# Performance work log

Hardware: AMD Instinct MI355X
Metric: run time of the kernel (lower is better)

The kernel has to match this reference:

```python
import jax, jax.numpy as jnp
import numpy as np

D_MODEL = 1024
NUM_HEADS = 16
D_K = D_MODEL // NUM_HEADS
S, B = 2048, 2


def setup_inputs() -> dict:
    key = jax.random.key(0)
    ks = jax.random.split(key, 11)
    lim = 1.0 / np.sqrt(D_MODEL)
    def lin(kw, kb):
        W = jax.random.uniform(kw, (D_MODEL, D_MODEL), jnp.float32, -lim, lim)
        b = jax.random.uniform(kb, (D_MODEL,), jnp.float32, -lim, lim)
        return W, b
    Wq, bq = lin(ks[0], ks[1])
    Wk, bk = lin(ks[2], ks[3])
    Wv, bv = lin(ks[4], ks[5])
    Wo, bo = lin(ks[6], ks[7])
    q = jax.random.normal(ks[8], (S, B, D_MODEL), jnp.float32)
    k = jax.random.normal(ks[9], (S, B, D_MODEL), jnp.float32)
    v = jax.random.normal(ks[10], (S, B, D_MODEL), jnp.float32)
    return {"q": q, "k": k, "v": v,
            "Wq": Wq, "bq": bq, "Wk": Wk, "bk": bk,
            "Wv": Wv, "bv": bv, "Wo": Wo, "bo": bo}


def reference(q, k, v, Wq, bq, Wk, bk, Wv, bv, Wo, bo):
    s, b, _ = q.shape
    scale = np.sqrt(D_K).astype(np.float32)
    # torch Linear: x @ W.T + b
    def proj(x, W, bias):
        y = jnp.einsum('sbd,ed->sbe', x, W) + bias
        # [S,B,D] -> [B,H,S,d_k]
        return y.reshape(s, b, NUM_HEADS, D_K).transpose(1, 2, 0, 3)
    Q = proj(q, Wq, bq)
    K = proj(k, Wk, bk)
    V = proj(v, Wv, bv)
    scores = jnp.einsum('bhsd,bhtd->bhst', Q, K) / scale  # [B,H,S,S]
    attn = jax.nn.softmax(scores, axis=-1)
    ctx = jnp.einsum('bhst,bhtd->bhsd', attn, V)  # [B,H,S,d_k]
    ctx = ctx.transpose(2, 0, 1, 3).reshape(s, b, NUM_HEADS * D_K)
    return jnp.einsum('sbd,ed->sbe', ctx, Wo) + bo
```

## Files before the change

kernel.cpp:

```cpp
#include <hip/hip_runtime.h>
#include <stdint.h>

typedef __attribute__((ext_vector_type(8))) short short8;
typedef __attribute__((ext_vector_type(4))) float f32x4;
typedef __attribute__((ext_vector_type(16))) float f32x16;

#define MFMA16(a, b, c) __builtin_amdgcn_mfma_f32_16x16x32_bf16((a), (b), (c), 0, 0, 0)
#define MFMA32(a, b, c) __builtin_amdgcn_mfma_f32_32x32x16_bf16((a), (b), (c), 0, 0, 0)

__device__ inline unsigned short f2bf(float x) {
  unsigned u = __float_as_uint(x);
  u = (u + 0x7FFFu + ((u >> 16) & 1u)) >> 16;
  return (unsigned short)u;
}

__device__ inline void gload16(const unsigned short* g, unsigned short* l) {
  __builtin_amdgcn_global_load_lds(
      (const __attribute__((address_space(1))) unsigned int*)g,
      (__attribute__((address_space(3))) unsigned int*)l, 16, 0, 0);
}

__device__ inline short8 lds8(const unsigned short* base, int byteoff) {
  return *reinterpret_cast<const short8*>(reinterpret_cast<const char*>(base) + byteoff);
}

__device__ inline unsigned cvtpk(float lo, float hi) {
  unsigned r;
  asm("v_cvt_pk_bf16_f32 %0, %1, %2" : "=v"(r) : "v"(lo), "v"(hi));
  return r;
}
__device__ inline void plswap(unsigned& a, unsigned& b) {
  asm volatile("v_permlane32_swap_b32 %0, %1" : "+v"(a), "+v"(b));
}
__device__ inline float swapadd(float v) {
  float a = v, b;
  asm volatile("v_mov_b32 %1, %0\n\tv_permlane32_swap_b32 %0, %1" : "+v"(a), "=&v"(b));
  return a + b;
}

__device__ inline short8 mk8(unsigned a, unsigned b, unsigned c, unsigned d) {
  union { unsigned u[4]; short8 v; } x;
  x.u[0] = a; x.u[1] = b; x.u[2] = c; x.u[3] = d;
  return x.v;
}

__device__ inline int swz(int row, int chunk) {
  return row * 128 + (((chunk) ^ (row & 7)) << 4);
}

__device__ inline void exppack(const f32x16& sv, float& lsum, short8& paLo, short8& paHi) {
  float p[16];
#pragma unroll
  for (int i = 0; i < 16; ++i) p[i] = __builtin_amdgcn_exp2f(sv[i]);
  float q8[8];
#pragma unroll
  for (int i = 0; i < 8; ++i) q8[i] = p[2 * i] + p[2 * i + 1];
#pragma unroll
  for (int s2 = 4; s2 > 0; s2 >>= 1)
#pragma unroll
    for (int i = 0; i < s2; ++i) q8[i] += q8[i + s2];
  lsum += q8[0];
  unsigned w0 = cvtpk(p[0], p[1]), w1 = cvtpk(p[2], p[3]);
  unsigned w2 = cvtpk(p[4], p[5]), w3 = cvtpk(p[6], p[7]);
  plswap(w0, w2); plswap(w1, w3);
  unsigned w4 = cvtpk(p[8], p[9]), w5 = cvtpk(p[10], p[11]);
  unsigned w6 = cvtpk(p[12], p[13]), w7 = cvtpk(p[14], p[15]);
  plswap(w4, w6); plswap(w5, w7);
  paLo = mk8(w0, w1, w2, w3);
  paHi = mk8(w4, w5, w6, w7);
}

__global__ __launch_bounds__(256) void cvt_bf16x(const float* __restrict__ a0,
                                                 const float* __restrict__ a1,
                                                 const float* __restrict__ a2,
                                                 const float* __restrict__ a3,
                                                 unsigned short* __restrict__ d, int per) {
  int y = blockIdx.y;
  const float* s = (y == 0) ? a0 : (y == 1) ? a1 : (y == 2) ? a2 : a3;
  int i = (blockIdx.x * 256 + threadIdx.x) * 8;
  if (i >= per) return;
  float4 v0 = *reinterpret_cast<const float4*>(s + i);
  float4 v1 = *reinterpret_cast<const float4*>(s + i + 4);
  short8 o;
  o[0] = (short)f2bf(v0.x); o[1] = (short)f2bf(v0.y);
  o[2] = (short)f2bf(v0.z); o[3] = (short)f2bf(v0.w);
  o[4] = (short)f2bf(v1.x); o[5] = (short)f2bf(v1.y);
  o[6] = (short)f2bf(v1.z); o[7] = (short)f2bf(v1.w);
  *reinterpret_cast<short8*>(d + (size_t)y * per + i) = o;
}

template <int MODE>
__global__ __launch_bounds__(256) void gemm_bt(
    const unsigned short* __restrict__ Abase, const unsigned short* __restrict__ Wbase,
    const float* __restrict__ bias0, const float* __restrict__ bias1,
    const float* __restrict__ bias2, unsigned short* __restrict__ ObaseBf,
    float* __restrict__ ObaseF, int M, int N, int K) {
  constexpr int CHUNK = (MODE == 0) ? 192 : 64;

  const int orig = blockIdx.x;
  const int wg = (orig & 7) * CHUNK + (orig >> 3);
  int z, bx, by;
  if (MODE == 0) {
    z = wg >> 9;
    int r = wg & 511;
    by = r & 15;
    bx = r >> 4;
  } else {
    z = 0; by = wg & 15; bx = wg >> 4;
  }

  const unsigned short* A = Abase + (size_t)z * M * K;
  const unsigned short* W = Wbase + (size_t)z * N * K;
  const float* bias = (z == 0) ? bias0 : (z == 1 ? bias1 : bias2);

  __shared__ unsigned short As[2 * 128 * 64];
  __shared__ unsigned short Bs[2 * 64 * 64];

  const int t = threadIdx.x;
  const int lane = t & 63, w = t >> 6;
  const int wm = w >> 1, wn = w & 1;
  const int m0 = bx * 128, n0 = by * 64;
  const int lrow = lane & 15, lg = lane >> 4;

  f32x4 acc[4][2] = {};

  int arow[4], acol[4], brow[2], bcol[2];
#pragma unroll
  for (int p = 0; p < 4; ++p) {
    int c = (p * 4 + w) * 64 + lane;
    arow[p] = c >> 3; acol[p] = ((c & 7) ^ (arow[p] & 7)) * 8;
  }
#pragma unroll
  for (int p = 0; p < 2; ++p) {
    int c = (p * 4 + w) * 64 + lane;
    brow[p] = c >> 3; bcol[p] = ((c & 7) ^ (brow[p] & 7)) * 8;
  }

#define STAGE_G(kt, buf)                                                              \
  {                                                                                   \
    _Pragma("unroll") for (int p = 0; p < 4; ++p)                                     \
        gload16(&A[(size_t)(m0 + arow[p]) * K + (kt) + acol[p]],                      \
                &As[(buf)*8192 + ((p * 4 + w) * 64) * 8]);                            \
    _Pragma("unroll") for (int p = 0; p < 2; ++p)                                     \
        gload16(&W[(size_t)(n0 + brow[p]) * K + (kt) + bcol[p]],                      \
                &Bs[(buf)*4096 + ((p * 4 + w) * 64) * 8]);                            \
  }

#define COMPUTE(buf)                                                                  \
  {                                                                                   \
    _Pragma("unroll") for (int kc = 0; kc < 2; ++kc) {                                \
      short8 af[4], bfr[2];                                                           \
      _Pragma("unroll") for (int i = 0; i < 4; ++i)                                   \
          af[i] = lds8(As, (buf)*16384 + swz(wm * 64 + i * 16 + lrow, kc * 4 + lg));  \
      _Pragma("unroll") for (int i = 0; i < 2; ++i)                                   \
          bfr[i] = lds8(Bs, (buf)*8192 + swz(wn * 32 + i * 16 + lrow, kc * 4 + lg));  \
      _Pragma("unroll") for (int mi = 0; mi < 4; ++mi)                                \
          _Pragma("unroll") for (int ni = 0; ni < 2; ++ni)                            \
              acc[mi][ni] = MFMA16(af[mi], bfr[ni], acc[mi][ni]);                     \
    }                                                                                 \
  }

  STAGE_G(0, 0);
  asm volatile("s_waitcnt vmcnt(0)" ::: "memory");
  __builtin_amdgcn_s_barrier();
  __builtin_amdgcn_sched_barrier(0);

  int cur = 0;
  for (int kt = 0; kt < K - 64; kt += 64) {
    STAGE_G(kt + 64, cur ^ 1);
    COMPUTE(cur);
    asm volatile("s_waitcnt vmcnt(0)" ::: "memory");
    __builtin_amdgcn_s_barrier();
    __builtin_amdgcn_sched_barrier(0);
    cur ^= 1;
  }
  COMPUTE(cur);
#undef STAGE_G
#undef COMPUTE

  const int r0 = lg * 4;
  if (MODE == 0) {
    const float scale = (z == 0) ? 0.18033688011112042f : 1.0f;
    if (z < 2) {
      unsigned short* O = ObaseBf + (size_t)z * (size_t)M * N;
#pragma unroll
      for (int mi = 0; mi < 4; ++mi)
#pragma unroll
        for (int ni = 0; ni < 2; ++ni) {
          int e = n0 + wn * 32 + ni * 16 + lrow;
          float be = bias[e];
          int h = e >> 6, d = e & 63;
#pragma unroll
          for (int r = 0; r < 4; ++r) {
            int m = m0 + wm * 64 + mi * 16 + r0 + r;
            int s = m >> 1, bb = m & 1;
            O[(((size_t)(bb * 16 + h) * 2048 + s) << 6) + d] = f2bf((acc[mi][ni][r] + be) * scale);
          }
        }
    } else {
      __builtin_amdgcn_s_barrier();
      unsigned short* T = As;
      const int h = n0 >> 6;
#pragma unroll
      for (int mi = 0; mi < 4; ++mi)
#pragma unroll
        for (int ni = 0; ni < 2; ++ni) {
          int d = wn * 32 + ni * 16 + lrow;
          float be = bias[n0 + d];
#pragma unroll
          for (int r = 0; r < 4; ++r) {
            int mrel = wm * 64 + mi * 16 + r0 + r;
            int sl = mrel >> 1, bb = mrel & 1;
            T[(bb * 64 + d) * 72 + sl] = f2bf(acc[mi][ni][r] + be);
          }
        }
      __builtin_amdgcn_s_barrier();
      unsigned short* O = ObaseBf + (size_t)2 * (size_t)M * N;
#pragma unroll
      for (int pass = 0; pass < 4; ++pass) {
        int rr = pass * 32 + (t >> 3);
        int sl8 = (t & 7) * 8;
        short8 vv = *reinterpret_cast<const short8*>(&T[rr * 72 + sl8]);
        int bb = rr >> 6, d = rr & 63;
        *reinterpret_cast<short8*>(
            &O[(((size_t)(bb * 16 + h) * 64 + d) << 11) + (m0 >> 1) + sl8]) = vv;
      }
    }
  } else {
    float* O = ObaseF;
#pragma unroll
    for (int mi = 0; mi < 4; ++mi)
#pragma unroll
      for (int ni = 0; ni < 2; ++ni) {
        int e = n0 + wn * 32 + ni * 16 + lrow;
        float be = bias[e];
#pragma unroll
        for (int r = 0; r < 4; ++r) {
          int m = m0 + wm * 64 + mi * 16 + r0 + r;
          O[(size_t)m * N + e] = acc[mi][ni][r] + be;
        }
      }
  }
}

__global__ __launch_bounds__(256, 2) void attn(const unsigned short* __restrict__ Q,
                                               const unsigned short* __restrict__ K,
                                               const unsigned short* __restrict__ Vt,
                                               unsigned short* __restrict__ ctx) {
  __shared__ unsigned short Ks[4 * 4096];
  __shared__ unsigned short Vs[4 * 4096];

  const int orig = blockIdx.x;
  const int wg = ((orig & 7) << 6) + (orig >> 3);
  const int bh = wg >> 4;
  const int qb = wg & 15;

  const int t = threadIdx.x, lane = t & 63, wv = t >> 6;
  const int q0 = qb * 128 + wv * 32;
  const int q = lane & 31, hi = lane >> 5;
  const int fq = (q ^ (q >> 3)) & 7;

  const unsigned short* Qb = Q + ((size_t)bh * 2048 + q0) * 64;
  const unsigned short* Kb = K + (size_t)bh * 2048 * 64;
  const unsigned short* Vb = Vt + (size_t)bh * 64 * 2048;

  short8 qf[4];
#pragma unroll
  for (int m = 0; m < 4; ++m)
    qf[m] = *reinterpret_cast<const short8*>(&Qb[q * 64 + m * 16 + hi * 8]);

  int koff[2][4], voff[2][2][2];
#pragma unroll
  for (int st = 0; st < 2; ++st) {
    int f = fq ^ (st ? 4 : 0);
#pragma unroll
    for (int m = 0; m < 4; ++m)
      koff[st][m] = (st * 32 + q) * 128 + (((m * 2 + hi) ^ f) << 4);
  }
#pragma unroll
  for (int dh = 0; dh < 2; ++dh) {
    int f = fq ^ (dh ? 4 : 0);
#pragma unroll
    for (int st = 0; st < 2; ++st)
#pragma unroll
      for (int kc = 0; kc < 2; ++kc)
        voff[dh][st][kc] = (dh * 32 + q) * 128 + (((st * 4 + kc * 2 + hi) ^ f) << 4);
  }

  int c0 = wv * 64 + lane, c1 = (4 + wv) * 64 + lane;
  int sr0 = c0 >> 3, sr1 = c1 >> 3;
  int sc0c = ((c0 & 7) ^ ((sr0 ^ (sr0 >> 3)) & 7)) * 8;
  int sc1c = ((c1 & 7) ^ ((sr1 ^ (sr1 >> 3)) & 7)) * 8;
  const unsigned short* ks0 = Kb + (size_t)sr0 * 64 + sc0c;
  const unsigned short* ks1 = Kb + (size_t)sr1 * 64 + sc1c;
  const unsigned short* vp0 = Vb + (size_t)sr0 * 2048 + sc0c;
  const unsigned short* vp1 = Vb + (size_t)sr1 * 2048 + sc1c;

#define STAGE(tt)                                                      \
  {                                                                    \
    char* kb = (char*)Ks + ((tt) & 3) * 8192;                          \
    char* vb2 = (char*)Vs + ((tt) & 3) * 8192;                         \
    gload16(ks0, (unsigned short*)(kb + wv * 1024));                   \
    gload16(ks1, (unsigned short*)(kb + (4 + wv) * 1024));             \
    gload16(vp0, (unsigned short*)(vb2 + wv * 1024));                  \
    gload16(vp1, (unsigned short*)(vb2 + (4 + wv) * 1024));            \
    ks0 += 4096; ks1 += 4096; vp0 += 64; vp1 += 64;                    \
  }

  f32x16 oa0 = {}, oa1 = {};
  float lsum = 0.f;
  const f32x16 zero16 = {};
  f32x16 sA0 = {}, sA1 = {}, sB0, sB1;

  STAGE(0); STAGE(1); STAGE(2);
  asm volatile("s_waitcnt vmcnt(8)" ::: "memory");
  __builtin_amdgcn_s_barrier();
  __builtin_amdgcn_sched_barrier(0);
#pragma unroll
  for (int m = 0; m < 4; ++m) {
    sA0 = MFMA32(lds8(Ks, koff[0][m]), qf[m], sA0);
    sA1 = MFMA32(lds8(Ks, koff[1][m]), qf[m], sA1);
  }

#define PHASE(tcur, sC0, sC1, sN0, sN1)                                         \
  {                                                                             \
    asm volatile("s_waitcnt vmcnt(4)" ::: "memory");                            \
    __builtin_amdgcn_sched_barrier(0);                                          \
    __builtin_amdgcn_s_barrier();                                               \
    __builtin_amdgcn_sched_barrier(0);                                          \
    STAGE((tcur) + 3);                                                          \
    sN0 = zero16; sN1 = zero16;                                                 \
    __builtin_amdgcn_s_setprio(1);                                              \
    {                                                                           \
      const int so = (((tcur) + 1) & 3) * 8192;                                 \
      _Pragma("unroll") for (int m = 0; m < 4; ++m) {                           \
        sN0 = MFMA32(lds8(Ks, so + koff[0][m]), qf[m], sN0);                    \
        sN1 = MFMA32(lds8(Ks, so + koff[1][m]), qf[m], sN1);                    \
      }                                                                         \
    }                                                                           \
    short8 paL0, paH0, paL1, paH1;                                              \
    exppack(sC0, lsum, paL0, paH0);                                             \
    exppack(sC1, lsum, paL1, paH1);                                             \
    {                                                                           \
      const int vo = ((tcur) & 3) * 8192;                                       \
      oa0 = MFMA32(paL0, lds8(Vs, vo + voff[0][0][0]), oa0);                    \
      oa1 = MFMA32(paL0, lds8(Vs, vo + voff[1][0][0]), oa1);                    \
      oa0 = MFMA32(paH0, lds8(Vs, vo + voff[0][0][1]), oa0);                    \
      oa1 = MFMA32(paH0, lds8(Vs, vo + voff[1][0][1]), oa1);                    \
      oa0 = MFMA32(paL1, lds8(Vs, vo + voff[0][1][0]), oa0);                    \
      oa1 = MFMA32(paL1, lds8(Vs, vo + voff[1][1][0]), oa1);                    \
      oa0 = MFMA32(paH1, lds8(Vs, vo + voff[0][1][1]), oa0);                    \
      oa1 = MFMA32(paH1, lds8(Vs, vo + voff[1][1][1]), oa1);                    \
    }                                                                           \
    __builtin_amdgcn_s_setprio(0);                                              \
  }

  for (int it = 0; it < 15; ++it) {
    int tc = 2 * it;
    PHASE(tc, sA0, sA1, sB0, sB1);
    PHASE(tc + 1, sB0, sB1, sA0, sA1);
  }
  PHASE(30, sA0, sA1, sB0, sB1);

  {
    short8 paL0, paH0, paL1, paH1;
    exppack(sB0, lsum, paL0, paH0);
    exppack(sB1, lsum, paL1, paH1);
    const int vo = 3 * 8192;
    oa0 = MFMA32(paL0, lds8(Vs, vo + voff[0][0][0]), oa0);
    oa1 = MFMA32(paL0, lds8(Vs, vo + voff[1][0][0]), oa1);
    oa0 = MFMA32(paH0, lds8(Vs, vo + voff[0][0][1]), oa0);
    oa1 = MFMA32(paH0, lds8(Vs, vo + voff[1][0][1]), oa1);
    oa0 = MFMA32(paL1, lds8(Vs, vo + voff[0][1][0]), oa0);
    oa1 = MFMA32(paL1, lds8(Vs, vo + voff[1][1][0]), oa1);
    oa0 = MFMA32(paH1, lds8(Vs, vo + voff[0][1][1]), oa0);
    oa1 = MFMA32(paH1, lds8(Vs, vo + voff[1][1][1]), oa1);
  }
#undef PHASE
#undef STAGE

  lsum = swapadd(lsum);
  float linv = 1.0f / lsum;
  const int b = bh >> 4, h = bh & 15;
#pragma unroll
  for (int r = 0; r < 16; ++r) {
    int qr = (r & 3) + 8 * (r >> 2) + 4 * hi;
    float li = __shfl(linv, qr);
    size_t base = ((size_t)(q0 + qr) * 2 + b) * 1024 + h * 64 + q;
    ctx[base] = f2bf(oa0[r] * li);
    ctx[base + 32] = f2bf(oa1[r] * li);
  }
}

extern "C" void kernel_launch(void* const* d_in, const int* in_sizes, int n_in, void* d_out,
                              int out_size, void* d_ws, size_t ws_size, hipStream_t stream) {
  const float* q  = (const float*)d_in[0];
  const float* k  = (const float*)d_in[1];
  const float* v  = (const float*)d_in[2];
  const float* Wq = (const float*)d_in[3];
  const float* bq = (const float*)d_in[4];
  const float* Wk = (const float*)d_in[5];
  const float* bk = (const float*)d_in[6];
  const float* Wv = (const float*)d_in[7];
  const float* bv = (const float*)d_in[8];
  const float* Wo = (const float*)d_in[9];
  const float* bo = (const float*)d_in[10];

  const size_t SZ_IN = 4194304;
  const size_t SZ_W  = 1048576;
  unsigned short* ws  = (unsigned short*)d_ws;
  unsigned short* xb  = ws;
  unsigned short* Wb  = xb + 3 * SZ_IN;
  unsigned short* QKV = Wb + 4 * SZ_W;
  unsigned short* ctx = QKV + 3 * SZ_IN;

  cvt_bf16x<<<dim3(SZ_IN / 2048, 3), 256, 0, stream>>>(q, k, v, v, xb, (int)SZ_IN);
  cvt_bf16x<<<dim3(SZ_W / 2048, 4), 256, 0, stream>>>(Wq, Wk, Wv, Wo, Wb, (int)SZ_W);

  gemm_bt<0><<<1536, 256, 0, stream>>>(xb, Wb, bq, bk, bv, QKV, nullptr, 4096, 1024, 1024);
  attn<<<512, 256, 0, stream>>>(QKV, QKV + SZ_IN, QKV + 2 * SZ_IN, ctx);
  gemm_bt<1><<<512, 256, 0, stream>>>(ctx, Wb + 3 * SZ_W, bo, bo, bo, nullptr,
                                      (float*)d_out, 4096, 1024, 1024);
}
```

Measured before the change: 118.3 us.

## Switch attention K/V pipeline to double-buffered 128-key tiles

Result: no change. 116.1 us (-1.8%).

```diff
diff --git a/kernel.cpp b/kernel.cpp
--- a/kernel.cpp
+++ b/kernel.cpp
@@ -247,8 +247,8 @@
                                                const unsigned short* __restrict__ K,
                                                const unsigned short* __restrict__ Vt,
                                                unsigned short* __restrict__ ctx) {
-  __shared__ unsigned short Ks[4 * 4096];
-  __shared__ unsigned short Vs[4 * 4096];
+  __shared__ unsigned short Ks[2 * 8192];
+  __shared__ unsigned short Vs[2 * 8192];
 
   const int orig = blockIdx.x;
   const int wg = ((orig & 7) << 6) + (orig >> 3);
@@ -269,115 +269,104 @@
   for (int m = 0; m < 4; ++m)
     qf[m] = *reinterpret_cast<const short8*>(&Qb[q * 64 + m * 16 + hi * 8]);
 
-  int koff[2][4], voff[2][2][2];
-#pragma unroll
-  for (int st = 0; st < 2; ++st) {
-    int f = fq ^ (st ? 4 : 0);
+  int koff[4][4];
+#pragma unroll
+  for (int st = 0; st < 4; ++st) {
+    int f = fq ^ ((st & 1) * 4);
 #pragma unroll
     for (int m = 0; m < 4; ++m)
       koff[st][m] = (st * 32 + q) * 128 + (((m * 2 + hi) ^ f) << 4);
   }
+  int voff[2][4][2];
 #pragma unroll
   for (int dh = 0; dh < 2; ++dh) {
-    int f = fq ^ (dh ? 4 : 0);
-#pragma unroll
-    for (int st = 0; st < 2; ++st)
-#pragma unroll
-      for (int kc = 0; kc < 2; ++kc)
-        voff[dh][st][kc] = (dh * 32 + q) * 128 + (((st * 4 + kc * 2 + hi) ^ f) << 4);
-  }
-
-  int c0 = wv * 64 + lane, c1 = (4 + wv) * 64 + lane;
-  int sr0 = c0 >> 3, sr1 = c1 >> 3;
-  int sc0c = ((c0 & 7) ^ ((sr0 ^ (sr0 >> 3)) & 7)) * 8;
-  int sc1c = ((c1 & 7) ^ ((sr1 ^ (sr1 >> 3)) & 7)) * 8;
-  const unsigned short* ks0 = Kb + (size_t)sr0 * 64 + sc0c;
-  const unsigned short* ks1 = Kb + (size_t)sr1 * 64 + sc1c;
-  const unsigned short* vp0 = Vb + (size_t)sr0 * 2048 + sc0c;
-  const unsigned short* vp1 = Vb + (size_t)sr1 * 2048 + sc1c;
-
-#define STAGE(tt)                                                      \
-  {                                                                    \
-    char* kb = (char*)Ks + ((tt) & 3) * 8192;                          \
-    char* vb2 = (char*)Vs + ((tt) & 3) * 8192;                         \
-    gload16(ks0, (unsigned short*)(kb + wv * 1024));                   \
-    gload16(ks1, (unsigned short*)(kb + (4 + wv) * 1024));             \
-    gload16(vp0, (unsigned short*)(vb2 + wv * 1024));                  \
-    gload16(vp1, (unsigned short*)(vb2 + (4 + wv) * 1024));            \
-    ks0 += 4096; ks1 += 4096; vp0 += 64; vp1 += 64;                    \
+    int g = fq ^ (dh * 4);
+#pragma unroll
+    for (int st = 0; st < 4; ++st)
+#pragma unroll
+      for (int kc = 0; kc < 2; ++kc) {
+        int cir = st * 4 + kc * 2 + hi;
+        int scir = (cir & 8) | ((cir & 7) ^ g);
+        voff[dh][st][kc] = (dh * 32 + q) * 256 + (scir << 4);
+      }
+  }
+
+  const unsigned short* ksp[4];
+  const unsigned short* vpp[4];
+#pragma unroll
+  for (int p = 0; p < 4; ++p) {
+    int c = (p * 4 + wv) * 64 + lane;
+    int kr = c >> 3, kcc = c & 7;
+    int gk = (kr ^ (kr >> 3)) & 7;
+    ksp[p] = Kb + (size_t)kr * 64 + (kcc ^ gk) * 8;
+    int vr = c >> 4, cir = c & 15;
+    int gv = (vr ^ (vr >> 3)) & 7;
+    int scir = (cir & 8) | ((cir & 7) ^ gv);
+    vpp[p] = Vb + (size_t)vr * 2048 + scir * 8;
+  }
+
+#define STAGE(buf)                                                           \
+  {                                                                          \
+    _Pragma("unroll") for (int p = 0; p < 4; ++p)                            \
+        gload16(ksp[p], &Ks[(buf)*8192 + ((p * 4 + wv) * 64) * 8]);          \
+    _Pragma("unroll") for (int p = 0; p < 4; ++p)                            \
+        gload16(vpp[p], &Vs[(buf)*8192 + ((p * 4 + wv) * 64) * 8]);          \
+    _Pragma("unroll") for (int p = 0; p < 4; ++p) { ksp[p] += 8192; vpp[p] += 128; } \
+  }
+
+#define QK(st, sv)                                                           \
+  {                                                                          \
+    _Pragma("unroll") for (int m = 0; m < 4; ++m)                            \
+        sv = MFMA32(lds8(Ks, cb + koff[st][m]), qf[m], sv);                  \
+  }
+
+#define PV(st, pl, ph)                                                       \
+  {                                                                          \
+    oa0 = MFMA32(pl, lds8(Vs, cb + voff[0][st][0]), oa0);                    \
+    oa1 = MFMA32(pl, lds8(Vs, cb + voff[1][st][0]), oa1);                    \
+    oa0 = MFMA32(ph, lds8(Vs, cb + voff[0][st][1]), oa0);                    \
+    oa1 = MFMA32(ph, lds8(Vs, cb + voff[1][st][1]), oa1);                    \
   }
 
   f32x16 oa0 = {}, oa1 = {};
   float lsum = 0.f;
-  const f32x16 zero16 = {};
-  f32x16 sA0 = {}, sA1 = {}, sB0, sB1;
-
-  STAGE(0); STAGE(1); STAGE(2);
-  asm volatile("s_waitcnt vmcnt(8)" ::: "memory");
+
+  STAGE(0);
+  asm volatile("s_waitcnt vmcnt(0)" ::: "memory");
   __builtin_amdgcn_s_barrier();
   __builtin_amdgcn_sched_barrier(0);
-#pragma unroll
-  for (int m = 0; m < 4; ++m) {
-    sA0 = MFMA32(lds8(Ks, koff[0][m]), qf[m], sA0);
-    sA1 = MFMA32(lds8(Ks, koff[1][m]), qf[m], sA1);
-  }
-
-#define PHASE(tcur, sC0, sC1, sN0, sN1)                                         \
-  {                                                                             \
-    asm volatile("s_waitcnt vmcnt(4)" ::: "memory");                            \
-    __builtin_amdgcn_sched_barrier(0);                                          \
-    __builtin_amdgcn_s_barrier();                                               \
-    __builtin_amdgcn_sched_barrier(0);                                          \
-    STAGE((tcur) + 3);                                                          \
-    sN0 = zero16; sN1 = zero16;                                                 \
-    __builtin_amdgcn_s_setprio(1);                                              \
-    {                                                                           \
-      const int so = (((tcur) + 1) & 3) * 8192;                                 \
-      _Pragma("unroll") for (int m = 0; m < 4; ++m) {                           \
-        sN0 = MFMA32(lds8(Ks, so + koff[0][m]), qf[m], sN0);                    \
-        sN1 = MFMA32(lds8(Ks, so + koff[1][m]), qf[m], sN1);                    \
-      }                                                                         \
-    }                                                                           \
-    short8 paL0, paH0, paL1, paH1;                                              \
-    exppack(sC0, lsum, paL0, paH0);                                             \
-    exppack(sC1, lsum, paL1, paH1);                                             \
-    {                                                                           \
-      const int vo = ((tcur) & 3) * 8192;                                       \
-      oa0 = MFMA32(paL0, lds8(Vs, vo + voff[0][0][0]), oa0);                    \
-      oa1 = MFMA32(paL0, lds8(Vs, vo + voff[1][0][0]), oa1);                    \
-      oa0 = MFMA32(paH0, lds8(Vs, vo + voff[0][0][1]), oa0);                    \
-      oa1 = MFMA32(paH0, lds8(Vs, vo + voff[1][0][1]), oa1);                    \
-      oa0 = MFMA32(paL1, lds8(Vs, vo + voff[0][1][0]), oa0);                    \
-      oa1 = MFMA32(paL1, lds8(Vs, vo + voff[1][1][0]), oa1);                    \
-      oa0 = MFMA32(paH1, lds8(Vs, vo + voff[0][1][1]), oa0);                    \
-      oa1 = MFMA32(paH1, lds8(Vs, vo + voff[1][1][1]), oa1);                    \
-    }                                                                           \
-    __builtin_amdgcn_s_setprio(0);                                              \
-  }
-
-  for (int it = 0; it < 15; ++it) {
-    int tc = 2 * it;
-    PHASE(tc, sA0, sA1, sB0, sB1);
-    PHASE(tc + 1, sB0, sB1, sA0, sA1);
-  }
-  PHASE(30, sA0, sA1, sB0, sB1);
-
-  {
-    short8 paL0, paH0, paL1, paH1;
-    exppack(sB0, lsum, paL0, paH0);
-    exppack(sB1, lsum, paL1, paH1);
-    const int vo = 3 * 8192;
-    oa0 = MFMA32(paL0, lds8(Vs, vo + voff[0][0][0]), oa0);
-    oa1 = MFMA32(paL0, lds8(Vs, vo + voff[1][0][0]), oa1);
-    oa0 = MFMA32(paH0, lds8(Vs, vo + voff[0][0][1]), oa0);
-    oa1 = MFMA32(paH0, lds8(Vs, vo + voff[1][0][1]), oa1);
-    oa0 = MFMA32(paL1, lds8(Vs, vo + voff[0][1][0]), oa0);
-    oa1 = MFMA32(paL1, lds8(Vs, vo + voff[1][1][0]), oa1);
-    oa0 = MFMA32(paH1, lds8(Vs, vo + voff[0][1][1]), oa0);
-    oa1 = MFMA32(paH1, lds8(Vs, vo + voff[1][1][1]), oa1);
-  }
-#undef PHASE
+
+  for (int tile = 0; tile < 16; ++tile) {
+    const int cb = (tile & 1) * 16384;
+    if (tile < 15) STAGE((tile & 1) ^ 1);
+
+    __builtin_amdgcn_s_setprio(1);
+    f32x16 s0 = {}, s1 = {}, s2 = {}, s3 = {};
+    short8 pl, ph;
+    QK(0, s0);
+    QK(1, s1);
+    exppack(s0, lsum, pl, ph);
+    PV(0, pl, ph);
+    QK(2, s2);
+    exppack(s1, lsum, pl, ph);
+    PV(1, pl, ph);
+    QK(3, s3);
+    exppack(s2, lsum, pl, ph);
+    PV(2, pl, ph);
+    exppack(s3, lsum, pl, ph);
+    PV(3, pl, ph);
+    __builtin_amdgcn_s_setprio(0);
+
+    if (tile < 15) {
+      asm volatile("s_waitcnt vmcnt(0)" ::: "memory");
+      __builtin_amdgcn_sched_barrier(0);
+      __builtin_amdgcn_s_barrier();
+      __builtin_amdgcn_sched_barrier(0);
+    }
+  }
 #undef STAGE
+#undef QK
+#undef PV
 
   lsum = swapadd(lsum);
   float linv = 1.0f / lsum;
```
